# Kernel tuning notes

Hardware: AMD Instinct MI355X
Metric: run time of the kernel (lower is better)

## Reference

```python
import jax, jax.numpy as jnp
import numpy as np

N_HEADS = 16


def setup_inputs() -> dict:
    key = jax.random.key(0)
    ks = jax.random.split(key, 4)
    B, S, D = 2, 2048, 1024
    x = jax.random.normal(ks[0], (B, S, D), dtype=jnp.float32)
    scale = 1.0 / np.sqrt(D)
    Wq = jax.random.normal(ks[1], (D, D), dtype=jnp.float32) * scale
    Wk = jax.random.normal(ks[2], (D, D), dtype=jnp.float32) * scale
    Wv = jax.random.normal(ks[3], (D, D), dtype=jnp.float32) * scale
    bq = jnp.zeros((D,), jnp.float32)
    bk = jnp.zeros((D,), jnp.float32)
    bv = jnp.zeros((D,), jnp.float32)
    return {"x": x, "Wq": Wq, "bq": bq, "Wk": Wk, "bk": bk, "Wv": Wv, "bv": bv}


def _split_heads(t, n_heads):
    B, S, D = t.shape
    return t.reshape(B, S, n_heads, D // n_heads).transpose(0, 2, 1, 3)  # [B,H,S,hd]


def reference(x, Wq, bq, Wk, bk, Wv, bv):
    H = N_HEADS
    Q = _split_heads(x @ Wq + bq, H)
    K = _split_heads(x @ Wk + bk, H)
    V = _split_heads(x @ Wv + bv, H)
    head_size = Q.shape[-1]
    scores = jnp.einsum("bhqd,bhkd->bhqk", Q, K) / jnp.sqrt(jnp.float32(head_size))
    probs = jax.nn.softmax(scores, axis=-1)  # dropout p=0.01 -> identity in eval
    out = jnp.einsum("bhqk,bhkd->bhqd", probs, V)
    B, _, S, hd = out.shape
    return out.transpose(0, 2, 1, 3).reshape(B, S, H * hd)
```

## Files before the change

### kernel.cpp

```cpp
#include <hip/hip_runtime.h>
#include <hip/hip_bf16.h>

typedef __bf16 bf16x8 __attribute__((ext_vector_type(8)));
typedef float f32x4 __attribute__((ext_vector_type(4)));

#define B_ 2
#define S_ 2048
#define D_ 1024
#define H_ 16
#define HD_ 64
#define NT_ (S_ / 64)

__global__ __launch_bounds__(256) void qkv_gemm(
    const float* __restrict__ X,
    const float* __restrict__ Wq, const float* __restrict__ bq,
    const float* __restrict__ Wk, const float* __restrict__ bk,
    const float* __restrict__ Wv, const float* __restrict__ bv,
    __bf16* __restrict__ Qw, __bf16* __restrict__ Kw, __bf16* __restrict__ VTw)
{
  const int z = blockIdx.z;
  const float* W; const float* bias; __bf16* outp; float mult;
  if (z == 0)      { W = Wq; bias = bq; outp = Qw;  mult = 0.125f * 1.44269504088896f; }
  else if (z == 1) { W = Wk; bias = bk; outp = Kw;  mult = 1.0f; }
  else             { W = Wv; bias = bv; outp = VTw; mult = 1.0f; }

  const int tid  = threadIdx.x;
  const int wave = tid >> 6, lane = tid & 63, ln = lane & 15, quad = lane >> 4;
  const int m0 = blockIdx.y * 128, n0 = blockIdx.x * 128;
  const int wm = (wave & 1) * 64, wn = (wave >> 1) * 64;

  __shared__ __bf16 Als[128 * 56];
  __shared__ __bf16 Bls[128 * 56];

  f32x4 acc[4][4] = {};

  for (int k0 = 0; k0 < D_; k0 += 32) {
    __syncthreads();
#pragma unroll
    for (int i = 0; i < 2; ++i) {
      int task = tid + 256 * i;
      int kc = task & 3, m = task >> 2;
      const float* xp = X + (size_t)(m0 + m) * D_ + k0 + kc * 8;
      f32x4 a0 = *(const f32x4*)(xp);
      f32x4 a1 = *(const f32x4*)(xp + 4);
      bf16x8 t;
#pragma unroll
      for (int j = 0; j < 4; ++j) { t[j] = (__bf16)a0[j]; t[4 + j] = (__bf16)a1[j]; }
      *(bf16x8*)(Als + m * 56 + kc * 8) = t;
    }
#pragma unroll
    for (int i = 0; i < 2; ++i) {
      int task = tid + 256 * i;
      int n = task & 127, kc = task >> 7;
      const float* wp = W + (size_t)(k0 + kc * 8) * D_ + n0 + n;
      bf16x8 t;
#pragma unroll
      for (int j = 0; j < 8; ++j) t[j] = (__bf16)wp[(size_t)j * D_];
      *(bf16x8*)(Bls + n * 56 + kc * 8) = t;
    }
    __syncthreads();

    bf16x8 af[4], bfr[4];
#pragma unroll
    for (int mt = 0; mt < 4; ++mt)
      af[mt] = *(const bf16x8*)(Als + (wm + mt * 16 + ln) * 56 + quad * 8);
#pragma unroll
    for (int nt = 0; nt < 4; ++nt)
      bfr[nt] = *(const bf16x8*)(Bls + (wn + nt * 16 + ln) * 56 + quad * 8);
#pragma unroll
    for (int mt = 0; mt < 4; ++mt)
#pragma unroll
      for (int nt = 0; nt < 4; ++nt)
        acc[mt][nt] = __builtin_amdgcn_mfma_f32_16x16x32_bf16(af[mt], bfr[nt], acc[mt][nt], 0, 0, 0);
  }

#pragma unroll
  for (int nt = 0; nt < 4; ++nt) {
    int n_g = n0 + wn + nt * 16 + ln;
    float bv_ = bias[n_g];
#pragma unroll
    for (int mt = 0; mt < 4; ++mt) {
#pragma unroll
      for (int r = 0; r < 4; ++r) {
        int m_g = m0 + wm + mt * 16 + quad * 4 + r;
        float c = (acc[mt][nt][r] + bv_) * mult;
        if (z < 2) {
          outp[(size_t)m_g * D_ + n_g] = (__bf16)c;
        } else {
          outp[(size_t)(m_g >> 11) * D_ * S_ + (size_t)n_g * S_ + (m_g & (S_ - 1))] = (__bf16)c;
        }
      }
    }
  }
}

__global__ __launch_bounds__(512) void attn(
    const __bf16* __restrict__ Q, const __bf16* __restrict__ K,
    const __bf16* __restrict__ VT, float* __restrict__ out)
{
  const int tid  = threadIdx.x;
  const int wave = tid >> 6, lane = tid & 63, ln = lane & 15, quad = lane >> 4;

  const int f = blockIdx.x;
  const int xcd = f & 7, g = f >> 3;
  const int bh = ((g & 3) << 3) | xcd;
  const int qt = g >> 2;
  const int b = bh >> 4, h = bh & 15;

  const __bf16* Qp = Q + (size_t)(b * S_ + qt * 128 + wave * 16 + ln) * D_ + h * HD_ + quad * 8;
  bf16x8 qa[2];
  qa[0] = *(const bf16x8*)(Qp);
  qa[1] = *(const bf16x8*)(Qp + 32);

  const int r = tid >> 3, c = tid & 7;
  const __bf16* Kh = K + (size_t)b * S_ * D_ + h * HD_;
  const __bf16* Vh = VT + (size_t)(b * D_ + h * HD_) * S_;
  const __bf16* Kst = Kh + (size_t)r * D_ + c * 8;
  const __bf16* Vst = Vh + (size_t)r * S_ + c * 8;

  __shared__ __bf16 Kls[2][64 * 72];
  __shared__ __bf16 Vls[2][64 * 72];
  __shared__ __bf16 Pls[8][16 * 72];
  __bf16* Pw = Pls[wave];

  f32x4 acc[4] = {};
  float lpart[4] = {0.f, 0.f, 0.f, 0.f};

  bf16x8 kreg = *(const bf16x8*)(Kst);
  bf16x8 vreg = *(const bf16x8*)(Vst);

  for (int kt = 0; kt < NT_; ++kt) {
    __bf16* Kb = Kls[kt & 1];
    __bf16* Vb = Vls[kt & 1];
    *(bf16x8*)(Kb + r * 72 + c * 8) = kreg;
    *(bf16x8*)(Vb + r * 72 + c * 8) = vreg;
    if (kt + 1 < NT_) {
      kreg = *(const bf16x8*)(Kst + (size_t)(kt + 1) * 64 * D_);
      vreg = *(const bf16x8*)(Vst + (kt + 1) * 64);
    }
    __syncthreads();

    f32x4 sc[4] = {};
#pragma unroll
    for (int nt = 0; nt < 4; ++nt) {
#pragma unroll
      for (int ks = 0; ks < 2; ++ks) {
        bf16x8 kb = *(const bf16x8*)(Kb + (nt * 16 + ln) * 72 + ks * 32 + quad * 8);
        sc[nt] = __builtin_amdgcn_mfma_f32_16x16x32_bf16(qa[ks], kb, sc[nt], 0, 0, 0);
      }
    }

#pragma unroll
    for (int nt = 0; nt < 4; ++nt)
#pragma unroll
      for (int r2 = 0; r2 < 4; ++r2) {
        float p = __builtin_amdgcn_exp2f(sc[nt][r2]);
        lpart[r2] += p;
        Pw[(quad * 4 + r2) * 72 + nt * 16 + ln] = (__bf16)p;
      }

#pragma unroll
    for (int ks = 0; ks < 2; ++ks) {
      bf16x8 pa = *(const bf16x8*)(Pw + ln * 72 + ks * 32 + quad * 8);
#pragma unroll
      for (int dt = 0; dt < 4; ++dt) {
        bf16x8 vb = *(const bf16x8*)(Vb + (dt * 16 + ln) * 72 + ks * 32 + quad * 8);
        acc[dt] = __builtin_amdgcn_mfma_f32_16x16x32_bf16(pa, vb, acc[dt], 0, 0, 0);
      }
    }
    __syncthreads();
  }

#pragma unroll
  for (int off = 1; off <= 8; off <<= 1)
#pragma unroll
    for (int r2 = 0; r2 < 4; ++r2)
      lpart[r2] += __shfl_xor(lpart[r2], off);

  float inv[4];
#pragma unroll
  for (int r2 = 0; r2 < 4; ++r2) inv[r2] = 1.0f / lpart[r2];

#pragma unroll
  for (int dt = 0; dt < 4; ++dt) {
#pragma unroll
    for (int r2 = 0; r2 < 4; ++r2) {
      float o = acc[dt][r2] * inv[r2];
      out[(size_t)(b * S_ + qt * 128 + wave * 16 + quad * 4 + r2) * D_ + h * HD_ + dt * 16 + ln] = o;
    }
  }
}

extern "C" void kernel_launch(void* const* d_in, const int* in_sizes, int n_in,
                              void* d_out, int out_size, void* d_ws, size_t ws_size,
                              hipStream_t stream) {
  const float* X  = (const float*)d_in[0];
  const float* Wq = (const float*)d_in[1];
  const float* bq = (const float*)d_in[2];
  const float* Wk = (const float*)d_in[3];
  const float* bk = (const float*)d_in[4];
  const float* Wv = (const float*)d_in[5];
  const float* bv = (const float*)d_in[6];

  __bf16* Qw  = (__bf16*)d_ws;
  __bf16* Kw  = Qw + (size_t)B_ * S_ * D_;
  __bf16* VTw = Kw + (size_t)B_ * S_ * D_;
  float* out = (float*)d_out;

  qkv_gemm<<<dim3(8, 32, 3), 256, 0, stream>>>(X, Wq, bq, Wk, bk, Wv, bv, Qw, Kw, VTw);
  attn<<<512, 512, 0, stream>>>(Qw, Kw, VTw, out);
}
```

Measured before the change: 191.0 us.

## Pre-convert X and transpose weights to bf16, load GEMM tiles via global_load_lds

```diff
diff --git a/kernel.cpp b/kernel.cpp
--- a/kernel.cpp
+++ b/kernel.cpp
@@ -11,26 +11,81 @@
 #define HD_ 64
 #define NT_ (S_ / 64)
 
+__device__ inline void load_lds16(const __bf16* g, __bf16* l) {
+  __builtin_amdgcn_global_load_lds(
+      (const __attribute__((address_space(1))) void*)g,
+      (__attribute__((address_space(3))) void*)l, 16, 0, 0);
+}
+
+__global__ __launch_bounds__(256) void prep(
+    const float* __restrict__ X,
+    const float* __restrict__ Wq, const float* __restrict__ Wk,
+    const float* __restrict__ Wv,
+    __bf16* __restrict__ Xb, __bf16* __restrict__ WT)
+{
+  const int z = blockIdx.z, t = threadIdx.x;
+  if (z == 3) {
+    size_t base = ((size_t)(blockIdx.y * 16 + blockIdx.x)) * 16384 + t * 4;
+#pragma unroll
+    for (int i = 0; i < 16; ++i) {
+      size_t idx = base + (size_t)i * 1024;
+      f32x4 v = *(const f32x4*)(X + idx);
+      __bf16 o[4];
+#pragma unroll
+      for (int j = 0; j < 4; ++j) o[j] = (__bf16)v[j];
+      *(ulong1*)(Xb + idx) = *(ulong1*)o;
+    }
+    return;
+  }
+  const float* W = (z == 0) ? Wq : (z == 1) ? Wk : Wv;
+  __bf16* WTz = WT + (size_t)z * D_ * D_;
+  const int k0 = blockIdx.y * 64, n0 = blockIdx.x * 64;
+
+  __shared__ __bf16 T[64 * 72];
+  {
+    int kl = t >> 2, cg = (t & 3) * 16;
+    const float* wp = W + (size_t)(k0 + kl) * D_ + n0 + cg;
+    bf16x8 a, b;
+#pragma unroll
+    for (int j = 0; j < 4; ++j) { a[j] = (__bf16)wp[j];     a[4 + j] = (__bf16)wp[4 + j]; }
+#pragma unroll
+    for (int j = 0; j < 4; ++j) { b[j] = (__bf16)wp[8 + j]; b[4 + j] = (__bf16)wp[12 + j]; }
+    *(bf16x8*)(T + kl * 72 + cg) = a;
+    *(bf16x8*)(T + kl * 72 + cg + 8) = b;
+  }
+  __syncthreads();
+  {
+    int nl = t >> 2, kc = (t & 3) * 16;
+    bf16x8 a, b;
+#pragma unroll
+    for (int j = 0; j < 8; ++j) a[j] = T[(kc + j) * 72 + nl];
+#pragma unroll
+    for (int j = 0; j < 8; ++j) b[j] = T[(kc + 8 + j) * 72 + nl];
+    __bf16* op = WTz + (size_t)(n0 + nl) * D_ + k0 + kc;
+    *(bf16x8*)(op) = a;
+    *(bf16x8*)(op + 8) = b;
+  }
+}
+
 __global__ __launch_bounds__(256) void qkv_gemm(
-    const float* __restrict__ X,
-    const float* __restrict__ Wq, const float* __restrict__ bq,
-    const float* __restrict__ Wk, const float* __restrict__ bk,
-    const float* __restrict__ Wv, const float* __restrict__ bv,
+    const __bf16* __restrict__ Xb, const __bf16* __restrict__ WT,
+    const float* __restrict__ bq, const float* __restrict__ bk,
+    const float* __restrict__ bv,
     __bf16* __restrict__ Qw, __bf16* __restrict__ Kw, __bf16* __restrict__ VTw)
 {
   const int z = blockIdx.z;
-  const float* W; const float* bias; __bf16* outp; float mult;
-  if (z == 0)      { W = Wq; bias = bq; outp = Qw;  mult = 0.125f * 1.44269504088896f; }
-  else if (z == 1) { W = Wk; bias = bk; outp = Kw;  mult = 1.0f; }
-  else             { W = Wv; bias = bv; outp = VTw; mult = 1.0f; }
+  const __bf16* Wz = WT + (size_t)z * D_ * D_;
+  const float* bias = (z == 0) ? bq : (z == 1) ? bk : bv;
+  __bf16* outp = (z == 0) ? Qw : (z == 1) ? Kw : VTw;
+  const float mult = (z == 0) ? 0.125f * 1.44269504088896f : 1.0f;
 
   const int tid  = threadIdx.x;
   const int wave = tid >> 6, lane = tid & 63, ln = lane & 15, quad = lane >> 4;
   const int m0 = blockIdx.y * 128, n0 = blockIdx.x * 128;
   const int wm = (wave & 1) * 64, wn = (wave >> 1) * 64;
 
-  __shared__ __bf16 Als[128 * 56];
-  __shared__ __bf16 Bls[128 * 56];
+  __shared__ __bf16 Als[128 * 32];
+  __shared__ __bf16 Bls[128 * 32];
 
   f32x4 acc[4][4] = {};
 
@@ -38,35 +93,21 @@
     __syncthreads();
 #pragma unroll
     for (int i = 0; i < 2; ++i) {
-      int task = tid + 256 * i;
-      int kc = task & 3, m = task >> 2;
-      const float* xp = X + (size_t)(m0 + m) * D_ + k0 + kc * 8;
-      f32x4 a0 = *(const f32x4*)(xp);
-      f32x4 a1 = *(const f32x4*)(xp + 4);
-      bf16x8 t;
-#pragma unroll
-      for (int j = 0; j < 4; ++j) { t[j] = (__bf16)a0[j]; t[4 + j] = (__bf16)a1[j]; }
-      *(bf16x8*)(Als + m * 56 + kc * 8) = t;
-    }
-#pragma unroll
-    for (int i = 0; i < 2; ++i) {
-      int task = tid + 256 * i;
-      int n = task & 127, kc = task >> 7;
-      const float* wp = W + (size_t)(k0 + kc * 8) * D_ + n0 + n;
-      bf16x8 t;
-#pragma unroll
-      for (int j = 0; j < 8; ++j) t[j] = (__bf16)wp[(size_t)j * D_];
-      *(bf16x8*)(Bls + n * 56 + kc * 8) = t;
+      int cb = wave * 128 + i * 64;
+      int chunk = cb + lane;
+      int row = chunk >> 2, c = chunk & 3;
+      load_lds16(Xb + (size_t)(m0 + row) * D_ + k0 + c * 8, Als + cb * 8);
+      load_lds16(Wz + (size_t)(n0 + row) * D_ + k0 + c * 8, Bls + cb * 8);
     }
     __syncthreads();
 
     bf16x8 af[4], bfr[4];
 #pragma unroll
     for (int mt = 0; mt < 4; ++mt)
-      af[mt] = *(const bf16x8*)(Als + (wm + mt * 16 + ln) * 56 + quad * 8);
+      af[mt] = *(const bf16x8*)(Als + (wm + mt * 16 + ln) * 32 + quad * 8);
 #pragma unroll
     for (int nt = 0; nt < 4; ++nt)
-      bfr[nt] = *(const bf16x8*)(Bls + (wn + nt * 16 + ln) * 56 + quad * 8);
+      bfr[nt] = *(const bf16x8*)(Bls + (wn + nt * 16 + ln) * 32 + quad * 8);
 #pragma unroll
     for (int mt = 0; mt < 4; ++mt)
 #pragma unroll
@@ -203,10 +244,13 @@
   const float* bv = (const float*)d_in[6];
 
   __bf16* Qw  = (__bf16*)d_ws;
-  __bf16* Kw  = Qw + (size_t)B_ * S_ * D_;
-  __bf16* VTw = Kw + (size_t)B_ * S_ * D_;
+  __bf16* Kw  = Qw  + (size_t)B_ * S_ * D_;
+  __bf16* VTw = Kw  + (size_t)B_ * S_ * D_;
+  __bf16* Xb  = VTw + (size_t)B_ * S_ * D_;
+  __bf16* WT  = Xb  + (size_t)B_ * S_ * D_;
   float* out = (float*)d_out;
 
-  qkv_gemm<<<dim3(8, 32, 3), 256, 0, stream>>>(X, Wq, bq, Wk, bk, Wv, bv, Qw, Kw, VTw);
+  prep<<<dim3(16, 16, 4), 256, 0, stream>>>(X, Wq, Wk, Wv, Xb, WT);
+  qkv_gemm<<<dim3(8, 32, 3), 256, 0, stream>>>(Xb, WT, bq, bk, bv, Qw, Kw, VTw);
   attn<<<512, 512, 0, stream>>>(Qw, Kw, VTw, out);
 }
```

Measured after the change: 184.5 us. 3.4% less time.
